# Kernel optimization log

Hardware: AMD Instinct MI355X
Metric: run time of the kernel (lower is better)

The kernel has to match this reference:

```python
import jax, jax.numpy as jnp
import numpy as np

N_NODES = 50000
N_EDGES = 800000
IN_CH = 128
HID = 64
OUT_CH = 10
N_LAYERS = 5
N_GRAPHS = 128
BN_EPS = 1e-5


def setup_inputs() -> dict:
    key = jax.random.key(0)
    ks = jax.random.split(key, 20)
    s = 0.1
    inp = {}
    inp["x"] = jax.random.normal(ks[0], (N_NODES, IN_CH), jnp.float32)
    inp["edge_index"] = jax.random.randint(ks[1], (2, N_EDGES), 0, N_NODES, dtype=jnp.int32)
    inp["batch"] = jnp.sort(jax.random.randint(ks[2], (N_NODES,), 0, N_GRAPHS, dtype=jnp.int32))
    # GINConv MLPs: layer 0 maps IN_CH->HID->HID, layers 1..4 map HID->HID->HID
    inp["w1_0"] = jax.random.normal(ks[3], (IN_CH, HID), jnp.float32) * s
    inp["b1_0"] = jnp.zeros((HID,), jnp.float32)
    inp["w2_0"] = jax.random.normal(ks[4], (HID, HID), jnp.float32) * s
    inp["b2_0"] = jnp.zeros((HID,), jnp.float32)
    inp["w1_rest"] = jax.random.normal(ks[5], (N_LAYERS - 1, HID, HID), jnp.float32) * s
    inp["b1_rest"] = jnp.zeros((N_LAYERS - 1, HID), jnp.float32)
    inp["w2_rest"] = jax.random.normal(ks[6], (N_LAYERS - 1, HID, HID), jnp.float32) * s
    inp["b2_rest"] = jnp.zeros((N_LAYERS - 1, HID), jnp.float32)
    # JK 'cat' projection: Linear(N_LAYERS*HID -> HID)
    inp["jk_w"] = jax.random.normal(ks[7], (N_LAYERS * HID, HID), jnp.float32) * s
    inp["jk_b"] = jnp.zeros((HID,), jnp.float32)
    # classifier MLP([HID, HID, OUT]) with batch_norm between
    inp["clf_w1"] = jax.random.normal(ks[8], (HID, HID), jnp.float32) * s
    inp["clf_b1"] = jnp.zeros((HID,), jnp.float32)
    inp["bn_gamma"] = jnp.ones((HID,), jnp.float32)
    inp["bn_beta"] = jnp.zeros((HID,), jnp.float32)
    inp["clf_w2"] = jax.random.normal(ks[9], (HID, OUT_CH), jnp.float32) * s
    inp["clf_b2"] = jnp.zeros((OUT_CH,), jnp.float32)
    return inp


def reference(x, edge_index, batch, w1_0, b1_0, w2_0, b2_0,
              w1_rest, b1_rest, w2_rest, b2_rest, jk_w, jk_b,
              clf_w1, clf_b1, bn_gamma, bn_beta, clf_w2, clf_b2):
    src, dst = edge_index[0], edge_index[1]
    xs = []
    h = x
    for i in range(N_LAYERS):
        # GINConv: mlp((1+eps)*x + sum_{j in N(i)} x_j), eps=0
        agg = jax.ops.segment_sum(h[src], dst, num_segments=N_NODES)  # [N, d]
        z = agg + h
        if i == 0:
            w1, b1, w2, b2 = w1_0, b1_0, w2_0, b2_0
        else:
            w1, b1, w2, b2 = w1_rest[i - 1], b1_rest[i - 1], w2_rest[i - 1], b2_rest[i - 1]
        h = jax.nn.relu(z @ w1 + b1) @ w2 + b2
        # BasicGNN post-conv activation (dropout disabled in inference)
        h = jax.nn.relu(h)
        xs.append(h)
    # JumpingKnowledge 'cat' + projection back to HID
    h = jnp.concatenate(xs, axis=-1) @ jk_w + jk_b  # [N, HID]
    # global_add_pool: per-graph sum
    g = jax.ops.segment_sum(h, batch, num_segments=N_GRAPHS)  # [G, HID]
    # classifier MLP with batch_norm (batch statistics)
    t = g @ clf_w1 + clf_b1
    mu = t.mean(axis=0)
    var = ((t - mu) ** 2).mean(axis=0)
    t = (t - mu) * jax.lax.rsqrt(var + BN_EPS) * bn_gamma + bn_beta
    t = jax.nn.relu(t)
    return t @ clf_w2 + clf_b2  # [G, OUT]
```

## Files before the change

### kernel.cpp

```cpp
#include <hip/hip_runtime.h>
#include <hip/hip_fp16.h>

#define NN 50000
#define NE 800000
#define NG 128
#define OUTC 10
#define SCAN_NB ((NN + 255) / 256)
#define NTILE 3125

__global__ void count_kernel(const int* __restrict__ dst, int* __restrict__ cnt) {
  for (int e = blockIdx.x * blockDim.x + threadIdx.x; e < NE; e += gridDim.x * blockDim.x)
    atomicAdd(&cnt[dst[e]], 1);
}

__global__ __launch_bounds__(256) void partial_kernel(const int* __restrict__ cnt,
                                                      int* __restrict__ part) {
  __shared__ int red[256];
  const int t = threadIdx.x;
  const int idx = blockIdx.x * 256 + t;
  red[t] = (idx < NN) ? cnt[idx] : 0;
  __syncthreads();
#pragma unroll
  for (int off = 128; off > 0; off >>= 1) {
    if (t < off) red[t] += red[t + off];
    __syncthreads();
  }
  if (t == 0) part[blockIdx.x] = red[0];
}

__global__ __launch_bounds__(256) void scanpart_kernel(int* __restrict__ part) {
  __shared__ int s[256];
  const int t = threadIdx.x;
  s[t] = (t < SCAN_NB) ? part[t] : 0;
  __syncthreads();
#pragma unroll
  for (int off = 1; off < 256; off <<= 1) {
    const int v = (t >= off) ? s[t - off] : 0;
    __syncthreads();
    s[t] += v;
    __syncthreads();
  }
  if (t < SCAN_NB) part[t] = (t == 0) ? 0 : s[t - 1];
}

__global__ __launch_bounds__(256) void scatter_scan_kernel(const int* __restrict__ cnt,
                                                           const int* __restrict__ part,
                                                           int* __restrict__ rowptr,
                                                           int* __restrict__ cursor) {
  __shared__ int s[256];
  const int t = threadIdx.x;
  const int idx = blockIdx.x * 256 + t;
  s[t] = (idx < NN) ? cnt[idx] : 0;
  __syncthreads();
#pragma unroll
  for (int off = 1; off < 256; off <<= 1) {
    const int v = (t >= off) ? s[t - off] : 0;
    __syncthreads();
    s[t] += v;
    __syncthreads();
  }
  const int excl = part[blockIdx.x] + ((t == 0) ? 0 : s[t - 1]);
  if (idx < NN) { rowptr[idx] = excl; cursor[idx] = excl; }
  if (idx == 0) rowptr[NN] = NE;
}

__global__ void fill_kernel(const int* __restrict__ src, const int* __restrict__ dst,
                            int* __restrict__ cursor, int* __restrict__ esrc) {
  for (int e = blockIdx.x * blockDim.x + threadIdx.x; e < NE; e += gridDim.x * blockDim.x) {
    int p = atomicAdd(&cursor[dst[e]], 1);
    esrc[p] = src[e];
  }
}

__global__ __launch_bounds__(128) void gbounds_kernel(const int* __restrict__ batch,
                                                      float* __restrict__ gcnt) {
  __shared__ int sb[NG + 1];
  const int g = threadIdx.x;
  int lo = 0, hi = NN;
  while (lo < hi) {
    const int mid = (lo + hi) >> 1;
    if (batch[mid] < g) lo = mid + 1; else hi = mid;
  }
  sb[g] = lo;
  if (g == 0) sb[NG] = NN;
  __syncthreads();
  gcnt[g] = (float)(sb[g + 1] - sb[g]);
}

__global__ __launch_bounds__(256) void proj_kernel(const float* __restrict__ x,
                                                   const float* __restrict__ w1,
                                                   __half* __restrict__ y) {
  __shared__ float sW[128 * 64];
  __shared__ float sX[64 * 128];
  const int t = threadIdx.x, c = t & 63, rg = t >> 6;
  for (int i = t; i < 128 * 64; i += 256) sW[i] = w1[i];
  const int ntiles = (NN + 63) / 64;
  for (int tile = blockIdx.x; tile < ntiles; tile += gridDim.x) {
    const int r0 = tile * 64, nv = min(64, NN - r0);
    __syncthreads();
    for (int i = t; i < nv * 32; i += 256)
      ((float4*)sX)[i] = ((const float4*)(x + (size_t)r0 * 128))[i];
    __syncthreads();
    float acc[16];
#pragma unroll
    for (int i = 0; i < 16; ++i) acc[i] = 0.f;
    for (int k = 0; k < 128; k += 4) {
      const float w0 = sW[(k + 0) * 64 + c], w1v = sW[(k + 1) * 64 + c],
                  w2v = sW[(k + 2) * 64 + c], w3v = sW[(k + 3) * 64 + c];
#pragma unroll
      for (int i = 0; i < 16; ++i) {
        const float4 xv = *(const float4*)&sX[(rg * 16 + i) * 128 + k];
        acc[i] = fmaf(xv.x, w0, acc[i]);
        acc[i] = fmaf(xv.y, w1v, acc[i]);
        acc[i] = fmaf(xv.z, w2v, acc[i]);
        acc[i] = fmaf(xv.w, w3v, acc[i]);
      }
    }
#pragma unroll
    for (int i = 0; i < 16; ++i) {
      const int r = rg * 16 + i;
      if (r < nv) y[(size_t)(r0 + r) * 64 + c] = __float2half(acc[i]);
    }
  }
}

template <bool HASW1, bool WRITEH>
__global__ __launch_bounds__(256) void gin_fused_kernel(
    const __half* __restrict__ hin, const int* __restrict__ rowptr,
    const int* __restrict__ esrc,
    const float* __restrict__ w1, const float* __restrict__ b1,
    const float* __restrict__ w2, const float* __restrict__ b2,
    __half* __restrict__ hout, const int* __restrict__ batch,
    float* __restrict__ gl) {
  __shared__ float sS[4][16 * 64];
  const int t = threadIdx.x, c = t & 63, wv = t >> 6;
  const int wg = blockIdx.x * 4 + wv;
  if (wg >= NTILE) return;
  float* slice = &sS[wv][0];
  const int n0 = wg * 16;
  const int oct = c >> 3, i = c & 7;

  const int rA = n0 + 2 * oct;
  const int pA0 = rowptr[rA], pA1 = rowptr[rA + 1], pB1 = rowptr[rA + 2];
  union H8 { float4 f; __half2 h2[4]; };
  const __half* hch = hin + i * 8;
  float zA[8], zB[8];
  {
    H8 u0, u1;
    u0.f = *(const float4*)(hch + (size_t)rA * 64);
    u1.f = *(const float4*)(hch + (size_t)(rA + 1) * 64);
#pragma unroll
    for (int k = 0; k < 4; ++k) {
      const float2 f0 = __half22float2(u0.h2[k]);
      const float2 f1 = __half22float2(u1.h2[k]);
      zA[2 * k] = f0.x; zA[2 * k + 1] = f0.y;
      zB[2 * k] = f1.x; zB[2 * k + 1] = f1.y;
    }
  }
  int e = pA0;
  for (; e + 1 < pA1; e += 2) {
    const int s0 = esrc[e], s1 = esrc[e + 1];
    H8 u0, u1;
    u0.f = *(const float4*)(hch + (size_t)s0 * 64);
    u1.f = *(const float4*)(hch + (size_t)s1 * 64);
#pragma unroll
    for (int k = 0; k < 4; ++k) {
      const float2 f0 = __half22float2(u0.h2[k]);
      const float2 f1 = __half22float2(u1.h2[k]);
      zA[2 * k]     += f0.x + f1.x;
      zA[2 * k + 1] += f0.y + f1.y;
    }
  }
  if (e < pA1) {
    H8 u0; u0.f = *(const float4*)(hch + (size_t)esrc[e] * 64);
#pragma unroll
    for (int k = 0; k < 4; ++k) {
      const float2 f0 = __half22float2(u0.h2[k]);
      zA[2 * k] += f0.x; zA[2 * k + 1] += f0.y;
    }
  }
  e = pA1;
  for (; e + 1 < pB1; e += 2) {
    const int s0 = esrc[e], s1 = esrc[e + 1];
    H8 u0, u1;
    u0.f = *(const float4*)(hch + (size_t)s0 * 64);
    u1.f = *(const float4*)(hch + (size_t)s1 * 64);
#pragma unroll
    for (int k = 0; k < 4; ++k) {
      const float2 f0 = __half22float2(u0.h2[k]);
      const float2 f1 = __half22float2(u1.h2[k]);
      zB[2 * k]     += f0.x + f1.x;
      zB[2 * k + 1] += f0.y + f1.y;
    }
  }
  if (e < pB1) {
    H8 u0; u0.f = *(const float4*)(hch + (size_t)esrc[e] * 64);
#pragma unroll
    for (int k = 0; k < 4; ++k) {
      const float2 f0 = __half22float2(u0.h2[k]);
      zB[2 * k] += f0.x; zB[2 * k + 1] += f0.y;
    }
  }
  if (!HASW1) {
    const float4 blo = *(const float4*)(b1 + i * 8);
    const float4 bhi = *(const float4*)(b1 + i * 8 + 4);
    zA[0] = fmaxf(zA[0] + blo.x, 0.f); zA[1] = fmaxf(zA[1] + blo.y, 0.f);
    zA[2] = fmaxf(zA[2] + blo.z, 0.f); zA[3] = fmaxf(zA[3] + blo.w, 0.f);
    zA[4] = fmaxf(zA[4] + bhi.x, 0.f); zA[5] = fmaxf(zA[5] + bhi.y, 0.f);
    zA[6] = fmaxf(zA[6] + bhi.z, 0.f); zA[7] = fmaxf(zA[7] + bhi.w, 0.f);
    zB[0] = fmaxf(zB[0] + blo.x, 0.f); zB[1] = fmaxf(zB[1] + blo.y, 0.f);
    zB[2] = fmaxf(zB[2] + blo.z, 0.f); zB[3] = fmaxf(zB[3] + blo.w, 0.f);
    zB[4] = fmaxf(zB[4] + bhi.x, 0.f); zB[5] = fmaxf(zB[5] + bhi.y, 0.f);
    zB[6] = fmaxf(zB[6] + bhi.z, 0.f); zB[7] = fmaxf(zB[7] + bhi.w, 0.f);
  }
  {
    const float4 a0 = {zA[0], zA[1], zA[2], zA[3]};
    const float4 a1 = {zA[4], zA[5], zA[6], zA[7]};
    const float4 b0v = {zB[0], zB[1], zB[2], zB[3]};
    const float4 b1v_ = {zB[4], zB[5], zB[6], zB[7]};
    *(float4*)&slice[(2 * oct) * 64 + i * 8] = a0;
    *(float4*)&slice[(2 * oct) * 64 + i * 8 + 4] = a1;
    *(float4*)&slice[(2 * oct + 1) * 64 + i * 8] = b0v;
    *(float4*)&slice[(2 * oct + 1) * 64 + i * 8 + 4] = b1v_;
  }

  const float b1c = b1[c], b2c = b2[c];
  if (HASW1) {
    float acc[16];
#pragma unroll
    for (int r = 0; r < 16; ++r) acc[r] = b1c;
    for (int kc = 0; kc < 4; ++kc) {
      float wr[16];
#pragma unroll
      for (int j = 0; j < 16; ++j) wr[j] = w1[(kc * 16 + j) * 64 + c];
#pragma unroll
      for (int r = 0; r < 16; ++r) {
        const float* zp = &slice[r * 64 + kc * 16];
        const float4 za = *(const float4*)(zp + 0);
        const float4 zb = *(const float4*)(zp + 4);
        const float4 zc = *(const float4*)(zp + 8);
        const float4 zd = *(const float4*)(zp + 12);
        float a = acc[r];
        a = fmaf(za.x, wr[0], a);  a = fmaf(za.y, wr[1], a);
        a = fmaf(za.z, wr[2], a);  a = fmaf(za.w, wr[3], a);
        a = fmaf(zb.x, wr[4], a);  a = fmaf(zb.y, wr[5], a);
        a = fmaf(zb.z, wr[6], a);  a = fmaf(zb.w, wr[7], a);
        a = fmaf(zc.x, wr[8], a);  a = fmaf(zc.y, wr[9], a);
        a = fmaf(zc.z, wr[10], a); a = fmaf(zc.w, wr[11], a);
        a = fmaf(zd.x, wr[12], a); a = fmaf(zd.y, wr[13], a);
        a = fmaf(zd.z, wr[14], a); a = fmaf(zd.w, wr[15], a);
        acc[r] = a;
      }
    }
#pragma unroll
    for (int r = 0; r < 16; ++r) slice[r * 64 + c] = fmaxf(acc[r], 0.f);
  }

  float acc2[16];
#pragma unroll
  for (int r = 0; r < 16; ++r) acc2[r] = b2c;
  for (int kc = 0; kc < 4; ++kc) {
    float wr[16];
#pragma unroll
    for (int j = 0; j < 16; ++j) wr[j] = w2[(kc * 16 + j) * 64 + c];
#pragma unroll
    for (int r = 0; r < 16; ++r) {
      const float* hp = &slice[r * 64 + kc * 16];
      const float4 za = *(const float4*)(hp + 0);
      const float4 zb = *(const float4*)(hp + 4);
      const float4 zc = *(const float4*)(hp + 8);
      const float4 zd = *(const float4*)(hp + 12);
      float a = acc2[r];
      a = fmaf(za.x, wr[0], a);  a = fmaf(za.y, wr[1], a);
      a = fmaf(za.z, wr[2], a);  a = fmaf(za.w, wr[3], a);
      a = fmaf(zb.x, wr[4], a);  a = fmaf(zb.y, wr[5], a);
      a = fmaf(zb.z, wr[6], a);  a = fmaf(zb.w, wr[7], a);
      a = fmaf(zc.x, wr[8], a);  a = fmaf(zc.y, wr[9], a);
      a = fmaf(zc.z, wr[10], a); a = fmaf(zc.w, wr[11], a);
      a = fmaf(zd.x, wr[12], a); a = fmaf(zd.y, wr[13], a);
      a = fmaf(zd.z, wr[14], a); a = fmaf(zd.w, wr[15], a);
      acc2[r] = a;
    }
  }
  float pacc = 0.f;
  int cur = batch[n0];
#pragma unroll
  for (int r = 0; r < 16; ++r) {
    const float hval = fmaxf(acc2[r], 0.f);
    if (WRITEH) hout[(size_t)(n0 + r) * 64 + c] = __float2half(hval);
    const int b = batch[n0 + r];
    if (b != cur) {
      atomicAdd(&gl[(size_t)cur * 64 + c], pacc);
      pacc = 0.f;
      cur = b;
    }
    pacc += hval;
  }
  atomicAdd(&gl[(size_t)cur * 64 + c], pacc);
}

__global__ __launch_bounds__(64) void jk_fold_kernel(
    const float* __restrict__ g5, const float* __restrict__ gcnt,
    const float* __restrict__ jkw, const float* __restrict__ jkb,
    const float* __restrict__ w1, const float* __restrict__ b1,
    float* __restrict__ tmat) {
  __shared__ float sg[64];
  const int gi = blockIdx.x, c = threadIdx.x;
  float a = jkb[c] * gcnt[gi];
  for (int l = 0; l < 5; ++l) {
    const float* gv = &g5[(size_t)(l * NG + gi) * 64];
    const float* wv = &jkw[(size_t)l * 64 * 64];
#pragma unroll 8
    for (int k = 0; k < 64; ++k) a = fmaf(gv[k], wv[k * 64 + c], a);
  }
  sg[c] = a;
  __syncthreads();
  float tv = b1[c];
#pragma unroll 8
  for (int k = 0; k < 64; ++k) tv = fmaf(sg[k], w1[k * 64 + c], tv);
  tmat[gi * 64 + c] = tv;
}

__global__ __launch_bounds__(256) void bn_out_kernel(
    const float* __restrict__ tmat, const float* __restrict__ gamma,
    const float* __restrict__ beta, const float* __restrict__ w2,
    const float* __restrict__ b2, float* __restrict__ out) {
  __shared__ float sT[NG * 64];
  __shared__ float sW2[64 * OUTC];
  __shared__ float sMu[64], sRs[64];
  const int t = threadIdx.x;
  for (int i = t; i < NG * 64; i += 256) sT[i] = tmat[i];
  for (int i = t; i < 64 * OUTC; i += 256) sW2[i] = w2[i];
  __syncthreads();
  if (t < 64) {
    float s = 0.f;
    for (int gi = 0; gi < NG; ++gi) s += sT[gi * 64 + t];
    const float mu = s / NG;
    float v = 0.f;
    for (int gi = 0; gi < NG; ++gi) { const float d = sT[gi * 64 + t] - mu; v += d * d; }
    v /= NG;
    sMu[t] = mu;
    sRs[t] = rsqrtf(v + 1e-5f);
  }
  __syncthreads();
  for (int idx = t; idx < NG * 64; idx += 256) {
    const int cc = idx & 63;
    sT[idx] = fmaxf((sT[idx] - sMu[cc]) * sRs[cc] * gamma[cc] + beta[cc], 0.f);
  }
  __syncthreads();
  for (int idx = t; idx < NG * OUTC; idx += 256) {
    const int gi = idx / OUTC, o = idx % OUTC;
    float a = b2[o];
    for (int k = 0; k < 64; ++k) a = fmaf(sT[gi * 64 + k], sW2[k * OUTC + o], a);
    out[idx] = a;
  }
}

extern "C" void kernel_launch(void* const* d_in, const int* in_sizes, int n_in,
                              void* d_out, int out_size, void* d_ws, size_t ws_size,
                              hipStream_t stream) {
  const float* x     = (const float*)d_in[0];
  const int*   ei    = (const int*)d_in[1];
  const int*   batch = (const int*)d_in[2];
  const float* w1_0  = (const float*)d_in[3];
  const float* b1_0  = (const float*)d_in[4];
  const float* w2_0  = (const float*)d_in[5];
  const float* b2_0  = (const float*)d_in[6];
  const float* w1_r  = (const float*)d_in[7];
  const float* b1_r  = (const float*)d_in[8];
  const float* w2_r  = (const float*)d_in[9];
  const float* b2_r  = (const float*)d_in[10];
  const float* jk_w  = (const float*)d_in[11];
  const float* jk_b  = (const float*)d_in[12];
  const float* cw1   = (const float*)d_in[13];
  const float* cb1   = (const float*)d_in[14];
  const float* bng   = (const float*)d_in[15];
  const float* bnb   = (const float*)d_in[16];
  const float* cw2   = (const float*)d_in[17];
  const float* cb2   = (const float*)d_in[18];
  float* out = (float*)d_out;

  char* base = (char*)d_ws;
  size_t o = 0;
  auto take = [&](size_t n) { char* p = base + o; o = (o + n + 255) & ~(size_t)255; return p; };
  int*    cnt    = (int*)take((size_t)NN * 4);
  int*    rowptr = (int*)take((size_t)(NN + 1) * 4);
  int*    cursor = (int*)take((size_t)NN * 4);
  int*    part   = (int*)take((size_t)SCAN_NB * 4);
  int*    esrc   = (int*)take((size_t)NE * 4);
  __half* hA     = (__half*)take((size_t)NN * 64 * 2);
  __half* hB     = (__half*)take((size_t)NN * 64 * 2);
  float*  g5     = (float*)take((size_t)5 * NG * 64 * 4);
  float*  gcnt   = (float*)take((size_t)NG * 4);
  float*  tmat   = (float*)take((size_t)NG * 64 * 4);
  (void)ws_size; (void)in_sizes; (void)n_in; (void)out_size;

  hipMemsetAsync(cnt, 0, (size_t)NN * 4, stream);
  hipMemsetAsync(g5, 0, (size_t)5 * NG * 64 * 4, stream);

  const int* src = ei;
  const int* dst = ei + NE;
  count_kernel<<<1024, 256, 0, stream>>>(dst, cnt);
  partial_kernel<<<SCAN_NB, 256, 0, stream>>>(cnt, part);
  scanpart_kernel<<<1, 256, 0, stream>>>(part);
  scatter_scan_kernel<<<SCAN_NB, 256, 0, stream>>>(cnt, part, rowptr, cursor);
  fill_kernel<<<1024, 256, 0, stream>>>(src, dst, cursor, esrc);
  gbounds_kernel<<<1, 128, 0, stream>>>(batch, gcnt);

  const int GRID = (NTILE + 3) / 4;

  proj_kernel<<<512, 256, 0, stream>>>(x, w1_0, hB);
  gin_fused_kernel<false, true><<<GRID, 256, 0, stream>>>(
      hB, rowptr, esrc, nullptr, b1_0, w2_0, b2_0, hA, batch, g5);
  const __half* hin = hA;
  __half* hout = hB;
  for (int l = 1; l < 5; ++l) {
    if (l < 4) {
      gin_fused_kernel<true, true><<<GRID, 256, 0, stream>>>(
          hin, rowptr, esrc, w1_r + (size_t)(l - 1) * 64 * 64,
          b1_r + (size_t)(l - 1) * 64, w2_r + (size_t)(l - 1) * 64 * 64,
          b2_r + (size_t)(l - 1) * 64, hout, batch, g5 + (size_t)l * NG * 64);
    } else {
      gin_fused_kernel<true, false><<<GRID, 256, 0, stream>>>(
          hin, rowptr, esrc, w1_r + (size_t)(l - 1) * 64 * 64,
          b1_r + (size_t)(l - 1) * 64, w2_r + (size_t)(l - 1) * 64 * 64,
          b2_r + (size_t)(l - 1) * 64, hout, batch, g5 + (size_t)l * NG * 64);
    }
    __half* tmp = (__half*)hin;
    hin = hout;
    hout = tmp;
  }

  jk_fold_kernel<<<NG, 64, 0, stream>>>(g5, gcnt, jk_w, jk_b, cw1, cb1, tmat);
  bn_out_kernel<<<1, 256, 0, stream>>>(tmat, bng, bnb, cw2, cb2, out);
}
```

Baseline: 427.6 us.

## Halve GIN node tile to 8 per wave and partition CSR fill by destination

The fused GIN kernel now gives each wave 8 nodes instead of 16. Each 8-lane group aggregates a single node's neighbours, with the gather loop unrolled by 4, and the wave count doubles to expose more parallel gather latency. The cost is that each wave loads its weight columns for half as many rows, so weight reuse per wave drops. The CSR fill kernel is also restructured: each block scans a fixed edge chunk and handles only edges whose destination falls in one of 8 node ranges. This localizes the cursor atomics and esrc writes, but reads the dst array 8 times.

```diff
diff --git a/kernel.cpp b/kernel.cpp
--- a/kernel.cpp
+++ b/kernel.cpp
@@ -6,7 +6,9 @@
 #define NG 128
 #define OUTC 10
 #define SCAN_NB ((NN + 255) / 256)
-#define NTILE 3125
+#define NTILE8 6250
+#define NODES_PER_PART 6250
+#define FILL_CH 6250
 
 __global__ void count_kernel(const int* __restrict__ dst, int* __restrict__ cnt) {
   for (int e = blockIdx.x * blockDim.x + threadIdx.x; e < NE; e += gridDim.x * blockDim.x)
@@ -64,11 +66,20 @@
   if (idx == 0) rowptr[NN] = NE;
 }
 
-__global__ void fill_kernel(const int* __restrict__ src, const int* __restrict__ dst,
-                            int* __restrict__ cursor, int* __restrict__ esrc) {
-  for (int e = blockIdx.x * blockDim.x + threadIdx.x; e < NE; e += gridDim.x * blockDim.x) {
-    int p = atomicAdd(&cursor[dst[e]], 1);
-    esrc[p] = src[e];
+__global__ __launch_bounds__(256) void fill_kernel(const int* __restrict__ src,
+                                                   const int* __restrict__ dst,
+                                                   int* __restrict__ cursor,
+                                                   int* __restrict__ esrc) {
+  const int p = blockIdx.x & 7;
+  const int q = blockIdx.x >> 3;
+  const int lo = p * NODES_PER_PART, hi = lo + NODES_PER_PART;
+  const int e0 = q * FILL_CH, e1 = e0 + FILL_CH;
+  for (int e = e0 + threadIdx.x; e < e1; e += 256) {
+    const int d = dst[e];
+    if (d >= lo && d < hi) {
+      const int pos = atomicAdd(&cursor[d], 1);
+      esrc[pos] = src[e];
+    }
   }
 }
 
@@ -132,109 +143,79 @@
     const float* __restrict__ w2, const float* __restrict__ b2,
     __half* __restrict__ hout, const int* __restrict__ batch,
     float* __restrict__ gl) {
-  __shared__ float sS[4][16 * 64];
+  __shared__ float sS[4][8 * 64];
   const int t = threadIdx.x, c = t & 63, wv = t >> 6;
   const int wg = blockIdx.x * 4 + wv;
-  if (wg >= NTILE) return;
+  if (wg >= NTILE8) return;
   float* slice = &sS[wv][0];
-  const int n0 = wg * 16;
+  const int n0 = wg * 8;
   const int oct = c >> 3, i = c & 7;
 
-  const int rA = n0 + 2 * oct;
-  const int pA0 = rowptr[rA], pA1 = rowptr[rA + 1], pB1 = rowptr[rA + 2];
+  const int rA = n0 + oct;
+  const int p0 = rowptr[rA], p1 = rowptr[rA + 1];
   union H8 { float4 f; __half2 h2[4]; };
   const __half* hch = hin + i * 8;
-  float zA[8], zB[8];
+  float z[8];
   {
-    H8 u0, u1;
-    u0.f = *(const float4*)(hch + (size_t)rA * 64);
-    u1.f = *(const float4*)(hch + (size_t)(rA + 1) * 64);
+    H8 u; u.f = *(const float4*)(hch + (size_t)rA * 64);
+#pragma unroll
+    for (int k = 0; k < 4; ++k) {
+      const float2 f = __half22float2(u.h2[k]);
+      z[2 * k] = f.x; z[2 * k + 1] = f.y;
+    }
+  }
+  int e = p0;
+  for (; e + 3 < p1; e += 4) {
+    const int s0 = esrc[e], s1 = esrc[e + 1], s2 = esrc[e + 2], s3 = esrc[e + 3];
+    H8 u0, u1, u2, u3;
+    u0.f = *(const float4*)(hch + (size_t)s0 * 64);
+    u1.f = *(const float4*)(hch + (size_t)s1 * 64);
+    u2.f = *(const float4*)(hch + (size_t)s2 * 64);
+    u3.f = *(const float4*)(hch + (size_t)s3 * 64);
 #pragma unroll
     for (int k = 0; k < 4; ++k) {
       const float2 f0 = __half22float2(u0.h2[k]);
       const float2 f1 = __half22float2(u1.h2[k]);
-      zA[2 * k] = f0.x; zA[2 * k + 1] = f0.y;
-      zB[2 * k] = f1.x; zB[2 * k + 1] = f1.y;
-    }
-  }
-  int e = pA0;
-  for (; e + 1 < pA1; e += 2) {
-    const int s0 = esrc[e], s1 = esrc[e + 1];
-    H8 u0, u1;
-    u0.f = *(const float4*)(hch + (size_t)s0 * 64);
-    u1.f = *(const float4*)(hch + (size_t)s1 * 64);
+      const float2 f2 = __half22float2(u2.h2[k]);
+      const float2 f3 = __half22float2(u3.h2[k]);
+      z[2 * k]     += (f0.x + f1.x) + (f2.x + f3.x);
+      z[2 * k + 1] += (f0.y + f1.y) + (f2.y + f3.y);
+    }
+  }
+  for (; e < p1; ++e) {
+    H8 u0; u0.f = *(const float4*)(hch + (size_t)esrc[e] * 64);
 #pragma unroll
     for (int k = 0; k < 4; ++k) {
       const float2 f0 = __half22float2(u0.h2[k]);
-      const float2 f1 = __half22float2(u1.h2[k]);
-      zA[2 * k]     += f0.x + f1.x;
-      zA[2 * k + 1] += f0.y + f1.y;
-    }
-  }
-  if (e < pA1) {
-    H8 u0; u0.f = *(const float4*)(hch + (size_t)esrc[e] * 64);
-#pragma unroll
-    for (int k = 0; k < 4; ++k) {
-      const float2 f0 = __half22float2(u0.h2[k]);
-      zA[2 * k] += f0.x; zA[2 * k + 1] += f0.y;
-    }
-  }
-  e = pA1;
-  for (; e + 1 < pB1; e += 2) {
-    const int s0 = esrc[e], s1 = esrc[e + 1];
-    H8 u0, u1;
-    u0.f = *(const float4*)(hch + (size_t)s0 * 64);
-    u1.f = *(const float4*)(hch + (size_t)s1 * 64);
-#pragma unroll
-    for (int k = 0; k < 4; ++k) {
-      const float2 f0 = __half22float2(u0.h2[k]);
-      const float2 f1 = __half22float2(u1.h2[k]);
-      zB[2 * k]     += f0.x + f1.x;
-      zB[2 * k + 1] += f0.y + f1.y;
-    }
-  }
-  if (e < pB1) {
-    H8 u0; u0.f = *(const float4*)(hch + (size_t)esrc[e] * 64);
-#pragma unroll
-    for (int k = 0; k < 4; ++k) {
-      const float2 f0 = __half22float2(u0.h2[k]);
-      zB[2 * k] += f0.x; zB[2 * k + 1] += f0.y;
+      z[2 * k] += f0.x; z[2 * k + 1] += f0.y;
     }
   }
   if (!HASW1) {
     const float4 blo = *(const float4*)(b1 + i * 8);
     const float4 bhi = *(const float4*)(b1 + i * 8 + 4);
-    zA[0] = fmaxf(zA[0] + blo.x, 0.f); zA[1] = fmaxf(zA[1] + blo.y, 0.f);
-    zA[2] = fmaxf(zA[2] + blo.z, 0.f); zA[3] = fmaxf(zA[3] + blo.w, 0.f);
-    zA[4] = fmaxf(zA[4] + bhi.x, 0.f); zA[5] = fmaxf(zA[5] + bhi.y, 0.f);
-    zA[6] = fmaxf(zA[6] + bhi.z, 0.f); zA[7] = fmaxf(zA[7] + bhi.w, 0.f);
-    zB[0] = fmaxf(zB[0] + blo.x, 0.f); zB[1] = fmaxf(zB[1] + blo.y, 0.f);
-    zB[2] = fmaxf(zB[2] + blo.z, 0.f); zB[3] = fmaxf(zB[3] + blo.w, 0.f);
-    zB[4] = fmaxf(zB[4] + bhi.x, 0.f); zB[5] = fmaxf(zB[5] + bhi.y, 0.f);
-    zB[6] = fmaxf(zB[6] + bhi.z, 0.f); zB[7] = fmaxf(zB[7] + bhi.w, 0.f);
+    z[0] = fmaxf(z[0] + blo.x, 0.f); z[1] = fmaxf(z[1] + blo.y, 0.f);
+    z[2] = fmaxf(z[2] + blo.z, 0.f); z[3] = fmaxf(z[3] + blo.w, 0.f);
+    z[4] = fmaxf(z[4] + bhi.x, 0.f); z[5] = fmaxf(z[5] + bhi.y, 0.f);
+    z[6] = fmaxf(z[6] + bhi.z, 0.f); z[7] = fmaxf(z[7] + bhi.w, 0.f);
   }
   {
-    const float4 a0 = {zA[0], zA[1], zA[2], zA[3]};
-    const float4 a1 = {zA[4], zA[5], zA[6], zA[7]};
-    const float4 b0v = {zB[0], zB[1], zB[2], zB[3]};
-    const float4 b1v_ = {zB[4], zB[5], zB[6], zB[7]};
-    *(float4*)&slice[(2 * oct) * 64 + i * 8] = a0;
-    *(float4*)&slice[(2 * oct) * 64 + i * 8 + 4] = a1;
-    *(float4*)&slice[(2 * oct + 1) * 64 + i * 8] = b0v;
-    *(float4*)&slice[(2 * oct + 1) * 64 + i * 8 + 4] = b1v_;
+    const float4 a0 = {z[0], z[1], z[2], z[3]};
+    const float4 a1 = {z[4], z[5], z[6], z[7]};
+    *(float4*)&slice[oct * 64 + i * 8] = a0;
+    *(float4*)&slice[oct * 64 + i * 8 + 4] = a1;
   }
 
   const float b1c = b1[c], b2c = b2[c];
   if (HASW1) {
-    float acc[16];
-#pragma unroll
-    for (int r = 0; r < 16; ++r) acc[r] = b1c;
+    float acc[8];
+#pragma unroll
+    for (int r = 0; r < 8; ++r) acc[r] = b1c;
     for (int kc = 0; kc < 4; ++kc) {
       float wr[16];
 #pragma unroll
       for (int j = 0; j < 16; ++j) wr[j] = w1[(kc * 16 + j) * 64 + c];
 #pragma unroll
-      for (int r = 0; r < 16; ++r) {
+      for (int r = 0; r < 8; ++r) {
         const float* zp = &slice[r * 64 + kc * 16];
         const float4 za = *(const float4*)(zp + 0);
         const float4 zb = *(const float4*)(zp + 4);
@@ -253,18 +234,18 @@
       }
     }
 #pragma unroll
-    for (int r = 0; r < 16; ++r) slice[r * 64 + c] = fmaxf(acc[r], 0.f);
-  }
-
-  float acc2[16];
-#pragma unroll
-  for (int r = 0; r < 16; ++r) acc2[r] = b2c;
+    for (int r = 0; r < 8; ++r) slice[r * 64 + c] = fmaxf(acc[r], 0.f);
+  }
+
+  float acc2[8];
+#pragma unroll
+  for (int r = 0; r < 8; ++r) acc2[r] = b2c;
   for (int kc = 0; kc < 4; ++kc) {
     float wr[16];
 #pragma unroll
     for (int j = 0; j < 16; ++j) wr[j] = w2[(kc * 16 + j) * 64 + c];
 #pragma unroll
-    for (int r = 0; r < 16; ++r) {
+    for (int r = 0; r < 8; ++r) {
       const float* hp = &slice[r * 64 + kc * 16];
       const float4 za = *(const float4*)(hp + 0);
       const float4 zb = *(const float4*)(hp + 4);
@@ -285,7 +266,7 @@
   float pacc = 0.f;
   int cur = batch[n0];
 #pragma unroll
-  for (int r = 0; r < 16; ++r) {
+  for (int r = 0; r < 8; ++r) {
     const float hval = fmaxf(acc2[r], 0.f);
     if (WRITEH) hout[(size_t)(n0 + r) * 64 + c] = __float2half(hval);
     const int b = batch[n0 + r];
@@ -407,7 +388,7 @@
   fill_kernel<<<1024, 256, 0, stream>>>(src, dst, cursor, esrc);
   gbounds_kernel<<<1, 128, 0, stream>>>(batch, gcnt);
 
-  const int GRID = (NTILE + 3) / 4;
+  const int GRID = (NTILE8 + 3) / 4;
 
   proj_kernel<<<512, 256, 0, stream>>>(x, w1_0, hB);
   gin_fused_kernel<false, true><<<GRID, 256, 0, stream>>>(
```

New measurement: 558.8 us. 1.31x slower.
